# Kernel tuning notes

Measured on AMD Instinct MI355X. Metric: run time of the kernel, lower is better.

## Reference

```python
import jax, jax.numpy as jnp
import numpy as np

HEAD_SIZE = 64
BLOCK_SIZE = 4096
BATCH = 4


def setup_inputs() -> dict:
    key = jax.random.key(0)
    kx, kk, kq, kv = jax.random.split(key, 4)
    x = jax.random.normal(kx, (BATCH, BLOCK_SIZE, HEAD_SIZE), dtype=jnp.float32)
    s = HEAD_SIZE ** -0.5  # ~ torch default linear init scale
    Wk = jax.random.uniform(kk, (HEAD_SIZE, HEAD_SIZE), jnp.float32, -s, s)
    Wq = jax.random.uniform(kq, (HEAD_SIZE, HEAD_SIZE), jnp.float32, -s, s)
    Wv = jax.random.uniform(kv, (HEAD_SIZE, HEAD_SIZE), jnp.float32, -s, s)
    return {"x": x, "Wk": Wk, "Wq": Wq, "Wv": Wv}


def reference(x, Wk, Wq, Wv):
    # x: [B, T, C]; W*: [C, C] stored torch-style (out, in) -> y = x @ W.T
    B, T, C = x.shape
    k = x @ Wk.T  # [B, T, C]
    q = x @ Wq.T
    v = x @ Wv.T
    scores = jnp.einsum('btc,bsc->bts', q, k) * (C ** -0.5)  # [B, T, T]
    causal = jnp.tril(jnp.ones((T, T), dtype=bool))
    scores = jnp.where(causal, scores, -jnp.inf)
    weights = jax.nn.softmax(scores, axis=-1)
    out = jnp.einsum('bts,bsc->btc', weights, v)  # [B, T, C]
    return out
```

## Files before the change

### kernel.cpp

```cpp
#include <hip/hip_runtime.h>
#include <hip/hip_bf16.h>

typedef unsigned short u16;
typedef unsigned int u32;
typedef __bf16 bf16x8_t __attribute__((ext_vector_type(8)));
typedef float f32x4_t __attribute__((ext_vector_type(4)));

constexpr int Bb = 4;
constexpr int Tt = 4096;
constexpr int Dd = 64;
constexpr float QSCALE = 0.18033688011112042f;

__device__ __forceinline__ u16 f2bf(float f) {
  unsigned int u = __builtin_bit_cast(unsigned int, f);
  return (u16)((u + 0x7fffu + ((u >> 16) & 1u)) >> 16);
}
__device__ __forceinline__ u32 pk2(float a, float b) {
  return (u32)f2bf(a) | ((u32)f2bf(b) << 16);
}
__device__ __forceinline__ u32 pkt(float a, float b) {
  const u32 ua = __builtin_bit_cast(u32, a);
  const u32 ub = __builtin_bit_cast(u32, b);
  return (ua >> 16) | (ub & 0xFFFF0000u);
}
__device__ __forceinline__ bf16x8_t ld16(const u16* p) {
  int4 v = *(const int4*)p;
  return __builtin_bit_cast(bf16x8_t, v);
}
__device__ __forceinline__ f32x4_t mfma16(bf16x8_t a, bf16x8_t b, f32x4_t c) {
  return __builtin_amdgcn_mfma_f32_16x16x32_bf16(a, b, c, 0, 0, 0);
}

__global__ __launch_bounds__(256) void HeadV1_proj(
    const float* __restrict__ x, const float* __restrict__ Wk,
    const float* __restrict__ Wq, const float* __restrict__ Wv,
    u16* __restrict__ qS, u16* __restrict__ kS, u16* __restrict__ vS)
{
  __shared__ u16 xl[64][72];
  __shared__ u16 Wl[3][64][72];
  __shared__ u16 ylds[64][72];

  const int t = threadIdx.x;
  const int w = t >> 6, lane = t & 63, l15 = lane & 15, quad = lane >> 4;
  const int r0 = blockIdx.x * 64;
  const int b  = r0 >> 12;
  const int kt = (r0 & 4095) >> 6;
  const long tilebase = ((long)(b * 64 + kt)) * 4096;

  {
    const float* srcs[4] = {x + (long)r0 * 64, Wk, Wq, Wv};
    u16* dstl[4] = {&xl[0][0], &Wl[0][0][0], &Wl[1][0][0], &Wl[2][0][0]};
    #pragma unroll
    for (int mm = 0; mm < 4; mm++) {
      const float* s = srcs[mm];
      u16* d = dstl[mm];
      #pragma unroll
      for (int i = 0; i < 4; i++) {
        const int f4 = i * 256 + t;
        const int row = f4 >> 4, c4 = f4 & 15;
        float4 v = ((const float4*)(s + row * 64))[c4];
        uint2 pk;
        pk.x = pk2(v.x, v.y);
        pk.y = pk2(v.z, v.w);
        *(uint2*)(d + row * 72 + c4 * 4) = pk;
      }
    }
  }
  __syncthreads();

  bf16x8_t xf[2];
  #pragma unroll
  for (int kh = 0; kh < 2; kh++)
    xf[kh] = ld16(&xl[w * 16 + l15][kh * 32 + quad * 8]);

  u16* dsts[3];
  dsts[0] = kS + tilebase; dsts[1] = qS + tilebase; dsts[2] = vS + tilebase;

  #pragma unroll
  for (int m = 0; m < 3; m++) {
    float vals[4][4];
    #pragma unroll
    for (int g = 0; g < 4; g++) {
      f32x4_t acc = {0.f, 0.f, 0.f, 0.f};
      #pragma unroll
      for (int kh = 0; kh < 2; kh++) {
        bf16x8_t wf = ld16(&Wl[m][g * 16 + l15][kh * 32 + quad * 8]);
        acc = mfma16(xf[kh], wf, acc);
      }
      #pragma unroll
      for (int r = 0; r < 4; r++)
        vals[g][r] = (m == 1) ? acc[r] * QSCALE : acc[r];
    }
    #pragma unroll
    for (int g = 0; g < 4; g++)
      #pragma unroll
      for (int r = 0; r < 4; r++)
        ylds[w * 16 + quad * 4 + r][g * 16 + l15] = f2bf(vals[g][r]);
    __syncthreads();
    if (m < 2) {
      #pragma unroll
      for (int kk = 0; kk < 2; kk++) {
        bf16x8_t f = ld16(&ylds[w * 16 + l15][kk * 32 + quad * 8]);
        *(int4*)(dsts[m] + (w * 2 + kk) * 512 + lane * 8) = __builtin_bit_cast(int4, f);
      }
    } else {
      #pragma unroll
      for (int kk = 0; kk < 2; kk++) {
        u16 tmp[8];
        #pragma unroll
        for (int j = 0; j < 8; j++)
          tmp[j] = ylds[kk * 32 + quad * 8 + j][w * 16 + l15];
        *(int4*)(dsts[2] + (kk * 4 + w) * 512 + lane * 8) = *(const int4*)tmp;
      }
    }
    __syncthreads();
  }
}

__global__ __launch_bounds__(512, 4) void HeadV1_flash(
    const u16* __restrict__ qS, const u16* __restrict__ kS,
    const u16* __restrict__ vS, float* __restrict__ outg)
{
  __shared__ __align__(16) char smem[26624];
  u16  (*pT)[32][36]   = (u16 (*)[32][36])smem;
  float (*chk)[16][33] = (float (*)[16][33])smem;
  float (*stg)[68]     = (float (*)[68])(smem + 16896);
  float (*lst)[32]     = (float (*)[32])(smem + 25600);

  const int t    = threadIdx.x;
  const int w    = t >> 6;
  const int lane = t & 63;
  const int l15  = lane & 15;
  const int quad = lane >> 4;

  const int b = blockIdx.x & 3;
  const int u = blockIdx.x >> 2;
  const int j = (u < 64) ? u : (191 - u);
  const int qt64 = j >> 1;
  const int ql0  = (j & 1) * 32;
  const int qr0  = j * 32;
  const long base = (long)b * Tt * Dd;

  union { u32 u4[4]; bf16x8_t v; } uo;
  uo.u4[0] = uo.u4[1] = uo.u4[2] = uo.u4[3] = 0x3F803F80u;
  const bf16x8_t ones = uo.v;
  const f32x4_t zero4 = {0.f, 0.f, 0.f, 0.f};

  const u16* qtile = qS + ((long)(b * 64 + qt64)) * 4096 + lane * 8;
  bf16x8_t qfrag[2][2];
  #pragma unroll
  for (int ct = 0; ct < 2; ct++)
    #pragma unroll
    for (int kd = 0; kd < 2; kd++)
      qfrag[ct][kd] = ld16(qtile + ((ql0 / 16 + ct) * 2 + kd) * 512);

  f32x4_t O[4][2];
  #pragma unroll
  for (int a = 0; a < 4; a++)
    #pragma unroll
    for (int c = 0; c < 2; c++)
      O[a][c] = zero4;
  f32x4_t Lc[2] = {zero4, zero4};

  const int nk = (j >> 1) + 1;

  for (int kt = w; kt < nk; kt += 8) {
    const bool ismask = (kt == nk - 1);
    const int kv0 = kt * 64;
    const u16* ktile = kS + ((long)(b * 64 + kt)) * 4096 + lane * 8;
    const u16* vtile = vS + ((long)(b * 64 + kt)) * 4096 + lane * 8;

    #pragma unroll
    for (int kk = 0; kk < 2; kk++) {
      bf16x8_t vf[4];
      #pragma unroll
      for (int dt = 0; dt < 4; dt++)
        vf[dt] = ld16(vtile + (kk * 4 + dt) * 512);

      #pragma unroll
      for (int rtl = 0; rtl < 2; rtl++) {
        const int rt = kk * 2 + rtl;
        bf16x8_t kf0 = ld16(ktile + (rt * 2 + 0) * 512);
        bf16x8_t kf1 = ld16(ktile + (rt * 2 + 1) * 512);
        #pragma unroll
        for (int ct = 0; ct < 2; ct++) {
          f32x4_t acc = zero4;
          acc = mfma16(kf0, qfrag[ct][0], acc);
          acc = mfma16(kf1, qfrag[ct][1], acc);
          if (ismask) {
            const int kvl = kv0 + rt * 16 + quad * 4;
            const int qi  = qr0 + ct * 16 + l15;
            #pragma unroll
            for (int r = 0; r < 4; r++)
              if (kvl + r > qi) acc[r] = -1e30f;
          }
          const float p0 = __builtin_amdgcn_exp2f(acc[0]);
          const float p1 = __builtin_amdgcn_exp2f(acc[1]);
          const float p2 = __builtin_amdgcn_exp2f(acc[2]);
          const float p3 = __builtin_amdgcn_exp2f(acc[3]);
          uint2 pk;
          pk.x = pkt(p0, p1);
          pk.y = pkt(p2, p3);
          *(uint2*)&pT[w][ct * 16 + l15][rtl * 16 + quad * 4] = pk;
        }
      }
      #pragma unroll
      for (int ct = 0; ct < 2; ct++) {
        bf16x8_t pf = ld16(&pT[w][ct * 16 + l15][quad * 8]);
        #pragma unroll
        for (int dt = 0; dt < 4; dt++)
          O[dt][ct] = mfma16(vf[dt], pf, O[dt][ct]);
        Lc[ct] = mfma16(ones, pf, Lc[ct]);
      }
    }
  }

  if (quad == 0) {
    #pragma unroll
    for (int ct = 0; ct < 2; ct++)
      lst[w][ct * 16 + l15] = Lc[ct][0];
  }
  __syncthreads();

  #pragma unroll
  for (int dt = 0; dt < 4; dt++) {
    #pragma unroll
    for (int ct = 0; ct < 2; ct++)
      #pragma unroll
      for (int r = 0; r < 4; r++)
        chk[w][quad * 4 + r][ct * 16 + l15] = O[dt][ct][r];
    __syncthreads();
    {
      const int d2 = t >> 5, q = t & 31;
      float s = 0.f;
      #pragma unroll
      for (int w2 = 0; w2 < 8; w2++) s += chk[w2][d2][q];
      stg[q][dt * 16 + d2] = s;
    }
    __syncthreads();
  }

  {
    const int q = t >> 4, dg = t & 15;
    float L = 0.f;
    #pragma unroll
    for (int w2 = 0; w2 < 8; w2++) L += lst[w2][q];
    const float invL = 1.0f / L;
    float4 v = *(const float4*)&stg[q][dg * 4];
    v.x *= invL; v.y *= invL; v.z *= invL; v.w *= invL;
    *(float4*)(outg + base + (long)(qr0 + q) * 64 + dg * 4) = v;
  }
}

extern "C" void kernel_launch(void* const* d_in, const int* in_sizes, int n_in,
                              void* d_out, int out_size, void* d_ws, size_t ws_size,
                              hipStream_t stream) {
  (void)in_sizes; (void)n_in; (void)out_size; (void)ws_size;
  const float* x  = (const float*)d_in[0];
  const float* Wk = (const float*)d_in[1];
  const float* Wq = (const float*)d_in[2];
  const float* Wv = (const float*)d_in[3];
  float* out = (float*)d_out;
  u16* qw  = (u16*)d_ws;
  u16* kw  = qw + (size_t)Bb * Tt * Dd;
  u16* vw  = kw + (size_t)Bb * Tt * Dd;

  HeadV1_proj<<<(Bb * Tt) / 64, 256, 0, stream>>>(x, Wk, Wq, Wv, qw, kw, vw);
  HeadV1_flash<<<512, 512, 0, stream>>>(qw, kw, vw, out);
}
```

Before: 86.35 us.

## Split flash attention into single-wave KV-chunk partial kernel plus merge kernel

After: 100.1 us. 1.16x slower.

```diff
diff --git a/kernel.cpp b/kernel.cpp
--- a/kernel.cpp
+++ b/kernel.cpp
@@ -10,6 +10,7 @@
 constexpr int Tt = 4096;
 constexpr int Dd = 64;
 constexpr float QSCALE = 0.18033688011112042f;
+constexpr int NSLOT = Bb * 128 * 16;
 
 __device__ __forceinline__ u16 f2bf(float f) {
   unsigned int u = __builtin_bit_cast(unsigned int, f);
@@ -117,29 +118,26 @@
   }
 }
 
-__global__ __launch_bounds__(512, 4) void HeadV1_flash(
+__global__ __launch_bounds__(64, 4) void HeadV1_part(
     const u16* __restrict__ qS, const u16* __restrict__ kS,
-    const u16* __restrict__ vS, float* __restrict__ outg)
+    const u16* __restrict__ vS, float* __restrict__ Opart,
+    float* __restrict__ Lpart)
 {
-  __shared__ __align__(16) char smem[26624];
-  u16  (*pT)[32][36]   = (u16 (*)[32][36])smem;
-  float (*chk)[16][33] = (float (*)[16][33])smem;
-  float (*stg)[68]     = (float (*)[68])(smem + 16896);
-  float (*lst)[32]     = (float (*)[32])(smem + 25600);
-
-  const int t    = threadIdx.x;
-  const int w    = t >> 6;
-  const int lane = t & 63;
-  const int l15  = lane & 15;
-  const int quad = lane >> 4;
-
-  const int b = blockIdx.x & 3;
-  const int u = blockIdx.x >> 2;
-  const int j = (u < 64) ? u : (191 - u);
+  __shared__ u16 pT[32][36];
+
+  const int u = blockIdx.x;
+  const int b = u & 3;
+  const int j = (u >> 2) & 127;
+  const int c = u >> 9;
+  const int nk = (j >> 1) + 1;
+  const int nc = (nk + 3) >> 2;
+  if (c >= nc) return;
+
+  const int lane = threadIdx.x;
+  const int l15 = lane & 15, quad = lane >> 4;
   const int qt64 = j >> 1;
   const int ql0  = (j & 1) * 32;
   const int qr0  = j * 32;
-  const long base = (long)b * Tt * Dd;
 
   union { u32 u4[4]; bf16x8_t v; } uo;
   uo.u4[0] = uo.u4[1] = uo.u4[2] = uo.u4[3] = 0x3F803F80u;
@@ -158,13 +156,14 @@
   #pragma unroll
   for (int a = 0; a < 4; a++)
     #pragma unroll
-    for (int c = 0; c < 2; c++)
-      O[a][c] = zero4;
+    for (int cc = 0; cc < 2; cc++)
+      O[a][cc] = zero4;
   f32x4_t Lc[2] = {zero4, zero4};
 
-  const int nk = (j >> 1) + 1;
-
-  for (int kt = w; kt < nk; kt += 8) {
+  const int k0 = c * 4;
+  const int kend = (k0 + 4 < nk) ? (k0 + 4) : nk;
+
+  for (int kt = k0; kt < kend; ++kt) {
     const bool ismask = (kt == nk - 1);
     const int kv0 = kt * 64;
     const u16* ktile = kS + ((long)(b * 64 + kt)) * 4096 + lane * 8;
@@ -201,12 +200,12 @@
           uint2 pk;
           pk.x = pkt(p0, p1);
           pk.y = pkt(p2, p3);
-          *(uint2*)&pT[w][ct * 16 + l15][rtl * 16 + quad * 4] = pk;
+          *(uint2*)&pT[ct * 16 + l15][rtl * 16 + quad * 4] = pk;
         }
       }
       #pragma unroll
       for (int ct = 0; ct < 2; ct++) {
-        bf16x8_t pf = ld16(&pT[w][ct * 16 + l15][quad * 8]);
+        bf16x8_t pf = ld16(&pT[ct * 16 + l15][quad * 8]);
         #pragma unroll
         for (int dt = 0; dt < 4; dt++)
           O[dt][ct] = mfma16(vf[dt], pf, O[dt][ct]);
@@ -215,41 +214,54 @@
     }
   }
 
+  const long slot = (long)((b * 128 + j) * 16 + c);
+  float* Op = Opart + slot * 2048;
+  #pragma unroll
+  for (int dt = 0; dt < 4; dt++)
+    #pragma unroll
+    for (int ct = 0; ct < 2; ct++)
+      *(f32x4_t*)(Op + ((dt * 2 + ct) * 64 + lane) * 4) = O[dt][ct];
   if (quad == 0) {
-    #pragma unroll
-    for (int ct = 0; ct < 2; ct++)
-      lst[w][ct * 16 + l15] = Lc[ct][0];
+    Lpart[slot * 32 + l15]      = Lc[0][0];
+    Lpart[slot * 32 + 16 + l15] = Lc[1][0];
+  }
+}
+
+__global__ __launch_bounds__(256) void HeadV1_merge(
+    const float* __restrict__ Opart, const float* __restrict__ Lpart,
+    float* __restrict__ outg)
+{
+  __shared__ float Ls[32];
+  const int t = threadIdx.x;
+  const int lane = t & 63, w = t >> 6;
+  const int b = blockIdx.x & 3;
+  const int j = blockIdx.x >> 2;
+  const int nk = (j >> 1) + 1;
+  const int nc = (nk + 3) >> 2;
+  const long slotbase = (long)((b * 128 + j) * 16);
+
+  f32x4_t a0 = {0.f, 0.f, 0.f, 0.f}, a1 = {0.f, 0.f, 0.f, 0.f};
+  for (int c = 0; c < nc; ++c) {
+    const float* Op = Opart + (slotbase + c) * 2048;
+    a0 += *(const f32x4_t*)(Op + (w * 64 + lane) * 4);
+    a1 += *(const f32x4_t*)(Op + ((w + 4) * 64 + lane) * 4);
+  }
+  if (t < 32) {
+    float s = 0.f;
+    for (int c = 0; c < nc; ++c) s += Lpart[(slotbase + c) * 32 + t];
+    Ls[t] = s;
   }
   __syncthreads();
 
-  #pragma unroll
-  for (int dt = 0; dt < 4; dt++) {
-    #pragma unroll
-    for (int ct = 0; ct < 2; ct++)
-      #pragma unroll
-      for (int r = 0; r < 4; r++)
-        chk[w][quad * 4 + r][ct * 16 + l15] = O[dt][ct][r];
-    __syncthreads();
-    {
-      const int d2 = t >> 5, q = t & 31;
-      float s = 0.f;
-      #pragma unroll
-      for (int w2 = 0; w2 < 8; w2++) s += chk[w2][d2][q];
-      stg[q][dt * 16 + d2] = s;
-    }
-    __syncthreads();
-  }
-
-  {
-    const int q = t >> 4, dg = t & 15;
-    float L = 0.f;
-    #pragma unroll
-    for (int w2 = 0; w2 < 8; w2++) L += lst[w2][q];
-    const float invL = 1.0f / L;
-    float4 v = *(const float4*)&stg[q][dg * 4];
-    v.x *= invL; v.y *= invL; v.z *= invL; v.w *= invL;
-    *(float4*)(outg + base + (long)(qr0 + q) * 64 + dg * 4) = v;
-  }
+  const int ct = w & 1, dtA = w >> 1, dtB = dtA + 2;
+  const int q = ct * 16 + (lane & 15);
+  const int d0 = (lane >> 4) * 4;
+  const float invL = 1.0f / Ls[q];
+  float* outp = outg + ((long)b * Tt + (long)j * 32 + q) * Dd;
+  f32x4_t vA = a0 * invL;
+  f32x4_t vB = a1 * invL;
+  *(f32x4_t*)(outp + dtA * 16 + d0) = vA;
+  *(f32x4_t*)(outp + dtB * 16 + d0) = vB;
 }
 
 extern "C" void kernel_launch(void* const* d_in, const int* in_sizes, int n_in,
@@ -261,10 +273,13 @@
   const float* Wq = (const float*)d_in[2];
   const float* Wv = (const float*)d_in[3];
   float* out = (float*)d_out;
-  u16* qw  = (u16*)d_ws;
-  u16* kw  = qw + (size_t)Bb * Tt * Dd;
-  u16* vw  = kw + (size_t)Bb * Tt * Dd;
+  u16* qw = (u16*)d_ws;
+  u16* kw = qw + (size_t)Bb * Tt * Dd;
+  u16* vw = kw + (size_t)Bb * Tt * Dd;
+  float* Op = (float*)(vw + (size_t)Bb * Tt * Dd);
+  float* Lp = Op + (size_t)NSLOT * 2048;
 
   HeadV1_proj<<<(Bb * Tt) / 64, 256, 0, stream>>>(x, Wk, Wq, Wv, qw, kw, vw);
-  HeadV1_flash<<<512, 512, 0, stream>>>(qw, kw, vw, out);
-}
+  HeadV1_part<<<NSLOT, 64, 0, stream>>>(qw, kw, vw, Op, Lp);
+  HeadV1_merge<<<Bb * 128, 256, 0, stream>>>(Op, Lp, out);
+}
```

## Pair causal query tiles per block and split waves proportionally to work

Applied to the files above, without the earlier changes.

Result: faster. 84.59 us (-2.0%).

```diff
diff --git a/kernel.cpp b/kernel.cpp
--- a/kernel.cpp
+++ b/kernel.cpp
@@ -117,15 +117,15 @@
   }
 }
 
-__global__ __launch_bounds__(512, 4) void HeadV1_flash(
+__global__ __launch_bounds__(1024, 4) void HeadV1_flash(
     const u16* __restrict__ qS, const u16* __restrict__ kS,
     const u16* __restrict__ vS, float* __restrict__ outg)
 {
-  __shared__ __align__(16) char smem[26624];
+  __shared__ __align__(16) char smem[53248];
   u16  (*pT)[32][36]   = (u16 (*)[32][36])smem;
   float (*chk)[16][33] = (float (*)[16][33])smem;
-  float (*stg)[68]     = (float (*)[68])(smem + 16896);
-  float (*lst)[32]     = (float (*)[32])(smem + 25600);
+  float (*stg)[32][68] = (float (*)[32][68])(smem + 33792);
+  float (*lst)[32]     = (float (*)[32])(smem + 33792 + 17408);
 
   const int t    = threadIdx.x;
   const int w    = t >> 6;
@@ -133,9 +133,21 @@
   const int l15  = lane & 15;
   const int quad = lane >> 4;
 
-  const int b = blockIdx.x & 3;
-  const int u = blockIdx.x >> 2;
-  const int j = (u < 64) ? u : (191 - u);
+  const int b  = blockIdx.x & 3;
+  const int i  = blockIdx.x >> 2;
+  const int j1 = i, j2 = 127 - i;
+  const int nk1 = (j1 >> 1) + 1;
+  const int nk2 = (j2 >> 1) + 1;
+  int n1 = (16 * nk1 + 32) / 65;
+  if (n1 < 1) n1 = 1;
+  if (n1 > 15) n1 = 15;
+
+  const bool grp2 = (w >= n1);
+  const int j   = grp2 ? j2 : j1;
+  const int nk  = grp2 ? nk2 : nk1;
+  const int str = grp2 ? (16 - n1) : n1;
+  const int off = grp2 ? (w - n1) : w;
+
   const int qt64 = j >> 1;
   const int ql0  = (j & 1) * 32;
   const int qr0  = j * 32;
@@ -162,9 +174,7 @@
       O[a][c] = zero4;
   f32x4_t Lc[2] = {zero4, zero4};
 
-  const int nk = (j >> 1) + 1;
-
-  for (int kt = w; kt < nk; kt += 8) {
+  for (int kt = off; kt < nk; kt += str) {
     const bool ismask = (kt == nk - 1);
     const int kv0 = kt * 64;
     const u16* ktile = kS + ((long)(b * 64 + kt)) * 4096 + lane * 8;
@@ -231,24 +241,27 @@
         chk[w][quad * 4 + r][ct * 16 + l15] = O[dt][ct][r];
     __syncthreads();
     {
-      const int d2 = t >> 5, q = t & 31;
+      const int jsel = t >> 9, tt = t & 511;
+      const int d2 = tt >> 5, q = tt & 31;
+      const int lo = jsel ? n1 : 0, hi = jsel ? 16 : n1;
       float s = 0.f;
-      #pragma unroll
-      for (int w2 = 0; w2 < 8; w2++) s += chk[w2][d2][q];
-      stg[q][dt * 16 + d2] = s;
+      for (int w2 = lo; w2 < hi; w2++) s += chk[w2][d2][q];
+      stg[jsel][q][dt * 16 + d2] = s;
     }
     __syncthreads();
   }
 
   {
-    const int q = t >> 4, dg = t & 15;
+    const int jsel = t >> 9, tt = t & 511;
+    const int q = tt >> 4, dg = tt & 15;
+    const int lo = jsel ? n1 : 0, hi = jsel ? 16 : n1;
     float L = 0.f;
-    #pragma unroll
-    for (int w2 = 0; w2 < 8; w2++) L += lst[w2][q];
+    for (int w2 = lo; w2 < hi; w2++) L += lst[w2][q];
     const float invL = 1.0f / L;
-    float4 v = *(const float4*)&stg[q][dg * 4];
+    const int jj = jsel ? j2 : j1;
+    float4 v = *(const float4*)&stg[jsel][q][dg * 4];
     v.x *= invL; v.y *= invL; v.z *= invL; v.w *= invL;
-    *(float4*)(outg + base + (long)(qr0 + q) * 64 + dg * 4) = v;
+    *(float4*)(outg + base + (long)(jj * 32 + q) * 64 + dg * 4) = v;
   }
 }
 
@@ -266,5 +279,5 @@
   u16* vw  = kw + (size_t)Bb * Tt * Dd;
 
   HeadV1_proj<<<(Bb * Tt) / 64, 256, 0, stream>>>(x, Wk, Wq, Wv, qw, kw, vw);
-  HeadV1_flash<<<512, 512, 0, stream>>>(qw, kw, vw, out);
-}
+  HeadV1_flash<<<256, 1024, 0, stream>>>(qw, kw, vw, out);
+}
```
